# Kernel tuning notes

Hardware: AMD Instinct MI355X
Metric: run time of the kernel (lower is better)

The kernel has to match this reference:

```python
import jax, jax.numpy as jnp
import numpy as np

D_MODEL = 512
PROJ = 2 * D_MODEL  # 1024
N_STATES = 32
KSIZE = 4
LN_EPS = 1e-3  # keras LayerNormalization default epsilon


def setup_inputs() -> dict:
    key = jax.random.key(0)
    ks = jax.random.split(key, 16)
    B, L = 2, 2048
    s_in = 1.0 / np.sqrt(D_MODEL)
    s_pr = 1.0 / np.sqrt(PROJ)
    x = jax.random.normal(ks[0], (B, L, D_MODEL), dtype=jnp.float32)
    # LayerNorm params
    ln_gamma = jnp.ones((D_MODEL,), jnp.float32)
    ln_beta = jnp.zeros((D_MODEL,), jnp.float32)
    # dense1 / dense2: d_model -> proj
    W1 = jax.random.normal(ks[1], (D_MODEL, PROJ), jnp.float32) * s_in
    b1 = jnp.zeros((PROJ,), jnp.float32)
    W2 = jax.random.normal(ks[2], (D_MODEL, PROJ), jnp.float32) * s_in
    b2 = jnp.zeros((PROJ,), jnp.float32)
    # depthwise causal conv1d: kernel (K, 1, PROJ) in WIO layout, groups=PROJ
    conv_k = jax.random.normal(ks[3], (KSIZE, 1, PROJ), jnp.float32) * 0.5
    conv_b = jnp.zeros((PROJ,), jnp.float32)
    # SSM params
    A_log = jnp.log(jnp.broadcast_to(jnp.arange(1, N_STATES + 1, dtype=jnp.float32), (PROJ, N_STATES)))
    D_skip = jnp.ones((PROJ,), jnp.float32)
    WB = jax.random.normal(ks[4], (PROJ, N_STATES), jnp.float32) * s_pr
    bB = jnp.zeros((N_STATES,), jnp.float32)
    WC = jax.random.normal(ks[5], (PROJ, N_STATES), jnp.float32) * s_pr
    bC = jnp.zeros((N_STATES,), jnp.float32)
    Wd = jax.random.normal(ks[6], (PROJ, PROJ), jnp.float32) * s_pr
    bd = jnp.zeros((PROJ,), jnp.float32)
    # dense3: proj -> d_model
    W3 = jax.random.normal(ks[7], (PROJ, D_MODEL), jnp.float32) * s_pr
    b3 = jnp.zeros((D_MODEL,), jnp.float32)
    return dict(x=x, ln_gamma=ln_gamma, ln_beta=ln_beta, W1=W1, b1=b1, W2=W2, b2=b2,
                conv_k=conv_k, conv_b=conv_b, A_log=A_log, D_skip=D_skip,
                WB=WB, bB=bB, WC=WC, bC=bC, Wd=Wd, bd=bd, W3=W3, b3=b3)


def _layernorm(x, gamma, beta):
    mu = jnp.mean(x, axis=-1, keepdims=True)
    var = jnp.mean(jnp.square(x - mu), axis=-1, keepdims=True)
    return (x - mu) * jax.lax.rsqrt(var + LN_EPS) * gamma + beta


def _causal_dwconv(x, k, b):
    # x: [B,L,C], k: [K,1,C], depthwise causal conv (left-pad K-1)
    y = jax.lax.conv_general_dilated(
        x, k, window_strides=(1,), padding=[(KSIZE - 1, 0)],
        dimension_numbers=('NWC', 'WIO', 'NWC'), feature_group_count=PROJ)
    return y + b


def _selective_scan(u, delta, A, Bm, Cm, D_skip):
    # u, delta: [B,L,D]; A: [D,N]; Bm, Cm: [B,L,N]; D_skip: [D]
    deltaA = jnp.einsum('bld,dn->bldn', delta, A)                 # [B,L,D,N]
    deltaBu = jnp.einsum('bld,bld,bln->bldn', delta, u, Bm)        # [B,L,D,N]
    # shift deltaA left by one along L, zero at the end (pad trick in source)
    shifted = jnp.concatenate([deltaA[:, 1:], jnp.zeros_like(deltaA[:, :1])], axis=1)
    # reversed cumsum along L, then exp
    e = jnp.exp(jnp.flip(jnp.cumsum(jnp.flip(shifted, axis=1), axis=1), axis=1))
    xs = jnp.cumsum(deltaBu * e, axis=1) / (e + 1e-12)
    y = jnp.einsum('bldn,bln->bld', xs, Cm)
    return y + u * D_skip


def reference(x, ln_gamma, ln_beta, W1, b1, W2, b2, conv_k, conv_b,
              A_log, D_skip, WB, bB, WC, bC, Wd, bd, W3, b3):
    h = _layernorm(x, ln_gamma, ln_beta)
    x1 = h @ W1 + b1                      # [B,L,PROJ]
    x1 = _causal_dwconv(x1, conv_k, conv_b)
    x1 = jax.nn.silu(x1)
    A = -jnp.exp(A_log)                    # [PROJ,N]
    Cm = x1 @ WC + bC                      # [B,L,N]
    Bm = x1 @ WB + bB                      # [B,L,N]
    delta = jax.nn.softplus(x1 @ Wd + bd)  # [B,L,PROJ]
    y = _selective_scan(x1, delta, A, Bm, Cm, D_skip)
    x2 = jax.nn.silu(h @ W2 + b2)
    out = (y * x2) @ W3 + b3 + x           # residual; dropout is identity at inference
    return out
```

## Files before the change

### kernel.cpp

```cpp
#include <hip/hip_runtime.h>
#include <stdint.h>

#define L_SEQ 2048
#define BATCH 2
#define DMODEL 512
#define PROJ 1024
#define NST 32
#define NCATU 1088
#define ROWS (BATCH*L_SEQ)
#define THRESH 50.0f

typedef float f32x4 __attribute__((ext_vector_type(4)));
typedef short short8 __attribute__((ext_vector_type(8)));

__device__ inline float bf2f(unsigned short u){ uint32_t x=((uint32_t)u)<<16; float f; __builtin_memcpy(&f,&x,4); return f; }
__device__ inline unsigned short f2bf(float f){ uint32_t x; __builtin_memcpy(&x,&f,4); uint32_t r=x+0x7FFFu+((x>>16)&1u); return (unsigned short)(r>>16); }
__device__ inline float siluf(float x){ return x/(1.f+__expf(-x)); }
__device__ inline float softplusf(float x){ return x>20.f? x : log1pf(__expf(x)); }

#define AS1(p) ((const __attribute__((address_space(1))) void*)(p))
#define AS3(p) ((__attribute__((address_space(3))) void*)(p))

template<int N> __device__ inline void wait_vmcnt(){
  if constexpr (N==0)      asm volatile("s_waitcnt vmcnt(0)" ::: "memory");
  else if constexpr (N==4) asm volatile("s_waitcnt vmcnt(4)" ::: "memory");
  else if constexpr (N==8) asm volatile("s_waitcnt vmcnt(8)" ::: "memory");
  else                     asm volatile("s_waitcnt vmcnt(12)" ::: "memory");
}

__global__ __launch_bounds__(256)
void prep_ln_kernel(const float* __restrict__ W1, const float* __restrict__ b1,
                    const float* __restrict__ W2, const float* __restrict__ b2,
                    const float* __restrict__ Wd, const float* __restrict__ bd,
                    const float* __restrict__ WB, const float* __restrict__ bB,
                    const float* __restrict__ WC, const float* __restrict__ bC,
                    const float* __restrict__ W3,
                    unsigned short* __restrict__ W12t, unsigned short* __restrict__ Wcatt,
                    unsigned short* __restrict__ W3t, float* __restrict__ bias12,
                    float* __restrict__ biascat,
                    const float* __restrict__ x, const float* __restrict__ ln_g,
                    const float* __restrict__ ln_b, unsigned short* __restrict__ H)
{
  __shared__ float tile[32][33];
  int bid = blockIdx.x;
  int lx = threadIdx.x & 31, ly = threadIdx.x >> 5;
  if (bid < 1024) {
    int kt = bid & 15, nt = bid >> 4;
    int k0 = kt*32, n0 = nt*32;
    const float* S = (n0 < 1024) ? W1 : W2;
    int nc = (n0 < 1024) ? n0 : n0 - 1024;
#pragma unroll
    for (int i=0;i<4;i++)
      tile[ly+i*8][lx] = S[(size_t)(k0+ly+i*8)*1024 + nc + lx];
    __syncthreads();
#pragma unroll
    for (int i=0;i<4;i++)
      W12t[(size_t)(n0+ly+i*8)*512 + k0 + lx] = f2bf(tile[lx][ly+i*8]);
    return;
  }
  if (bid < 2112) {
    int t = bid - 1024;
    int kt = t & 31, nt = t >> 5;
    int k0 = kt*32, n0 = nt*32;
#pragma unroll
    for (int i=0;i<4;i++){
      int k = k0 + ly + i*8;
      float v;
      if (n0 < 1024)       v = Wd[(size_t)k*1024 + n0 + lx];
      else if (n0 == 1024) v = WB[(size_t)k*32 + lx];
      else                 v = WC[(size_t)k*32 + lx];
      tile[ly+i*8][lx] = v;
    }
    __syncthreads();
#pragma unroll
    for (int i=0;i<4;i++)
      Wcatt[(size_t)(n0+ly+i*8)*1024 + k0 + lx] = f2bf(tile[lx][ly+i*8]);
    return;
  }
  if (bid < 2624) {
    int t = bid - 2112;
    int kt = t & 31, nt = t >> 5;
    int k0 = kt*32, n0 = nt*32;
#pragma unroll
    for (int i=0;i<4;i++)
      tile[ly+i*8][lx] = W3[(size_t)(k0+ly+i*8)*512 + n0 + lx];
    __syncthreads();
#pragma unroll
    for (int i=0;i<4;i++)
      W3t[(size_t)(n0+ly+i*8)*1024 + k0 + lx] = f2bf(tile[lx][ly+i*8]);
    return;
  }
  if (bid < 2637) {
    int j = (bid - 2624)*256 + threadIdx.x;
    if (j < 2048) { bias12[j] = (j < 1024) ? b1[j] : b2[j-1024]; return; }
    j -= 2048;
    if (j < NCATU) biascat[j] = (j < 1024) ? bd[j] : (j < 1056) ? bB[j-1024] : bC[j-1056];
    return;
  }
  int row = (bid - 2637)*4 + (threadIdx.x >> 6);
  int lane = threadIdx.x & 63;
  const float4* xr = (const float4*)(x + (size_t)row*DMODEL);
  float4 v0 = xr[lane];
  float4 v1 = xr[lane+64];
  float s = v0.x+v0.y+v0.z+v0.w + v1.x+v1.y+v1.z+v1.w;
  float q = v0.x*v0.x+v0.y*v0.y+v0.z*v0.z+v0.w*v0.w
          + v1.x*v1.x+v1.y*v1.y+v1.z*v1.z+v1.w*v1.w;
#pragma unroll
  for (int m=32;m>0;m>>=1){ s += __shfl_xor(s,m); q += __shfl_xor(q,m); }
  float mu = s*(1.f/DMODEL);
  float var = q*(1.f/DMODEL) - mu*mu;
  float rs = rsqrtf(var + 1e-3f);
  int c0 = lane*4, c1 = 256 + lane*4;
  float4 g0 = *(const float4*)&ln_g[c0]; float4 g1 = *(const float4*)&ln_g[c1];
  float4 t0 = *(const float4*)&ln_b[c0]; float4 t1 = *(const float4*)&ln_b[c1];
  ushort4 o0, o1;
  o0.x = f2bf((v0.x-mu)*rs*g0.x + t0.x);
  o0.y = f2bf((v0.y-mu)*rs*g0.y + t0.y);
  o0.z = f2bf((v0.z-mu)*rs*g0.z + t0.z);
  o0.w = f2bf((v0.w-mu)*rs*g0.w + t0.w);
  o1.x = f2bf((v1.x-mu)*rs*g1.x + t1.x);
  o1.y = f2bf((v1.y-mu)*rs*g1.y + t1.y);
  o1.z = f2bf((v1.z-mu)*rs*g1.z + t1.z);
  o1.w = f2bf((v1.w-mu)*rs*g1.w + t1.w);
  *(ushort4*)&H[(size_t)row*DMODEL + c0] = o0;
  *(ushort4*)&H[(size_t)row*DMODEL + c1] = o1;
}

template<int MODE>
__global__ __launch_bounds__(256)
void gemm64(const unsigned short* __restrict__ A, const unsigned short* __restrict__ Bt,
            void* __restrict__ Cv, void* __restrict__ Cv2, const float* __restrict__ bias,
            int M, int N, int K, int Kfull)
{
  constexpr int BK = 64;
  constexpr int LPT = 4;
  __shared__ unsigned short As[3][64*BK];
  __shared__ unsigned short Bs[3][64*BK];
  int tid = threadIdx.x;
  int lane = tid & 63, wid = tid >> 6;
  int wm = wid >> 1, wn = wid & 1;
  int gx = gridDim.x;
  int nwg = gx * gridDim.y;
  int L = blockIdx.y*gx + blockIdx.x;
  int W = (L & 7)*(nwg >> 3) + (L >> 3);
  int bx = W % gx, by = W / gx;
  int m0 = bx*64, n0 = by*64;
  int kofs = blockIdx.z*K;

  f32x4 acc[2][2];
#pragma unroll
  for (int i=0;i<2;i++)
#pragma unroll
    for (int j=0;j<2;j++)
#pragma unroll
      for (int e=0;e<4;e++) acc[i][j][e] = 0.f;

  const unsigned short* ap[2];
  const unsigned short* bp[2];
#pragma unroll
  for (int j=0;j<2;j++){
    int s = tid + j*256;
    int row = s >> 3, kc = ((s & 7) ^ (row & 7)) * 8;
    ap[j] = A + (size_t)(m0+row)*Kfull + kofs + kc;
    bp[j] = Bt + (size_t)(n0+row)*Kfull + kofs + kc;
  }
  auto stage = [&](int buf){
#pragma unroll
    for (int j=0;j<2;j++){
      __builtin_amdgcn_global_load_lds(AS1(ap[j]), AS3(&As[buf][(size_t)(j*256 + wid*64)*8]), 16, 0, 0);
      ap[j] += BK;
    }
#pragma unroll
    for (int j=0;j<2;j++){
      __builtin_amdgcn_global_load_lds(AS1(bp[j]), AS3(&Bs[buf][(size_t)(j*256 + wid*64)*8]), 16, 0, 0);
      bp[j] += BK;
    }
  };
  stage(0); stage(1);
  int T = K/BK;
  int rb = 0, wb = 2;
  int r = lane & 15, kb = lane >> 4;
  for (int t = 0; t < T; ++t) {
    if (t+1 < T) wait_vmcnt<LPT>();
    else         wait_vmcnt<0>();
    __builtin_amdgcn_s_barrier();
    if (t+2 < T) { stage(wb); wb = (wb==2)?0:wb+1; }
#pragma unroll
    for (int ks=0; ks<2; ++ks) {
      int cx = (ks*4 + kb) ^ (r & 7);
      short8 af[2], bfr[2];
#pragma unroll
      for (int i=0;i<2;i++) af[i]  = *(const short8*)&As[rb][((wm*32 + i*16 + r)*8 + cx)*8];
#pragma unroll
      for (int j=0;j<2;j++) bfr[j] = *(const short8*)&Bs[rb][((wn*32 + j*16 + r)*8 + cx)*8];
      __builtin_amdgcn_s_setprio(1);
#pragma unroll
      for (int i=0;i<2;i++)
#pragma unroll
        for (int j=0;j<2;j++)
          acc[i][j] = __builtin_amdgcn_mfma_f32_16x16x32_bf16(af[i], bfr[j], acc[i][j], 0,0,0);
      __builtin_amdgcn_s_setprio(0);
    }
    rb = (rb==2)?0:rb+1;
  }
  int rr = (lane >> 4)*4, cc = lane & 15;
#pragma unroll
  for (int i=0;i<2;i++)
#pragma unroll
    for (int j=0;j<2;j++) {
      int col = n0 + wn*32 + j*16 + cc;
#pragma unroll
      for (int e=0;e<4;e++) {
        int row = m0 + wm*32 + i*16 + rr + e;
        float v = acc[i][j][e];
        if constexpr (MODE == 1) {
          v += bias[col];
          if (col < 1024) ((unsigned short*)Cv)[(size_t)row*1024 + col] = f2bf(v);
          else            ((unsigned short*)Cv2)[(size_t)row*1024 + col - 1024] = f2bf(siluf(v));
        } else if constexpr (MODE == 2) {
          v += bias[row];
          if (row < 1024) v = softplusf(v);
          ((float*)Cv)[(size_t)row*N + col] = v;
        } else {
          ((float*)Cv)[(size_t)blockIdx.z*M*N + (size_t)row*N + col] = v;
        }
      }
    }
}

__global__ __launch_bounds__(256)
void reduce_kernel(const float* __restrict__ P, const float* __restrict__ x,
                   const float* __restrict__ b3, float* __restrict__ out)
{
  size_t i = ((size_t)blockIdx.x*256 + threadIdx.x)*4;
  int col = (int)(i & 511);
  float4 a = *(const float4*)&P[i];
  float4 b = *(const float4*)&P[(size_t)ROWS*512 + i];
  float4 xv = *(const float4*)&x[i];
  float4 bv = *(const float4*)&b3[col];
  float4 o;
  o.x = a.x + b.x + xv.x + bv.x;
  o.y = a.y + b.y + xv.y + bv.y;
  o.z = a.z + b.z + xv.z + bv.z;
  o.w = a.w + b.w + xv.w + bv.w;
  *(float4*)&out[i] = o;
}

__global__ __launch_bounds__(256)
void conv_silu_kernel(const unsigned short* __restrict__ P12n, const float* __restrict__ ck,
                      const float* __restrict__ cb, unsigned short* __restrict__ ubf)
{
  int gid = blockIdx.x*256 + threadIdx.x;
  int c = (gid & 255)*4;
  int row = gid >> 8;
  int l = row & (L_SEQ-1);
  float4 bv = *(const float4*)&cb[c];
  float r0=bv.x, r1=bv.y, r2=bv.z, r3=bv.w;
#pragma unroll
  for (int t=0;t<4;t++){
    int lsrc = l - 3 + t;
    if (lsrc >= 0) {
      ushort4 xv = *(const ushort4*)&P12n[(size_t)(row-3+t)*1024 + c];
      float4 kv = *(const float4*)&ck[t*PROJ + c];
      r0 = fmaf(bf2f(xv.x),kv.x,r0);
      r1 = fmaf(bf2f(xv.y),kv.y,r1);
      r2 = fmaf(bf2f(xv.z),kv.z,r2);
      r3 = fmaf(bf2f(xv.w),kv.w,r3);
    }
  }
  ushort4 o;
  o.x=f2bf(siluf(r0)); o.y=f2bf(siluf(r1)); o.z=f2bf(siluf(r2)); o.w=f2bf(siluf(r3));
  *(ushort4*)&ubf[(size_t)row*PROJ + c] = o;
}

__global__ __launch_bounds__(256)
void utrans_kernel(const unsigned short* __restrict__ u, const unsigned short* __restrict__ x2,
                   unsigned short* __restrict__ uT, unsigned short* __restrict__ x2T)
{
  __shared__ unsigned short tile[32][33];
  const unsigned short* src = blockIdx.z ? x2 : u;
  unsigned short* dst = blockIdx.z ? x2T : uT;
  int r0 = blockIdx.x*32, c0 = blockIdx.y*32;
  int lx = threadIdx.x & 31, ly = threadIdx.x >> 5;
#pragma unroll
  for (int i=0;i<4;i++)
    tile[ly+i*8][lx] = src[(size_t)(r0+ly+i*8)*1024 + c0 + lx];
  __syncthreads();
#pragma unroll
  for (int i=0;i<4;i++)
    dst[(size_t)(c0+ly+i*8)*ROWS + r0 + lx] = tile[lx][ly+i*8];
}

__global__ __launch_bounds__(256)
void zmul_pre_kernel(const unsigned short* __restrict__ ubf, const unsigned short* __restrict__ x2bf,
                     const float* __restrict__ Dskip, unsigned short* __restrict__ zbf)
{
  size_t i = ((size_t)blockIdx.x*256 + threadIdx.x)*4;
  int d = (int)(i & (PROJ-1));
  ushort4 uu = *(const ushort4*)&ubf[i];
  ushort4 xx = *(const ushort4*)&x2bf[i];
  float4 Dv = *(const float4*)&Dskip[d];
  ushort4 o;
  o.x = f2bf(bf2f(uu.x)*Dv.x*bf2f(xx.x));
  o.y = f2bf(bf2f(uu.y)*Dv.y*bf2f(xx.y));
  o.z = f2bf(bf2f(uu.z)*Dv.z*bf2f(xx.z));
  o.w = f2bf(bf2f(uu.w)*Dv.w*bf2f(xx.w));
  *(ushort4*)&zbf[i] = o;
}

__global__ __launch_bounds__(256)
void sscan_kernel(const float* __restrict__ CT, const unsigned short* __restrict__ uT,
                  const unsigned short* __restrict__ x2T, const float* __restrict__ Dskip,
                  const float* __restrict__ A_log, unsigned short* __restrict__ zbf)
{
  int tid = threadIdx.x;
  int lane = tid & 63;
  int G = blockIdx.x*4 + (tid >> 6);
  int b = G >> 10, d = G & 1023;
  const float* dT = CT + (size_t)d*ROWS + b*L_SEQ;

  float4 v4[8];
#pragma unroll
  for (int it=0; it<8; ++it) v4[it] = *(const float4*)&dT[lane*32 + it*4];
  float p1 = v4[0].x+v4[0].y+v4[0].z+v4[0].w + v4[1].x+v4[1].y+v4[1].z+v4[1].w;
  float p2 = p1 + v4[2].x+v4[2].y+v4[2].z+v4[2].w + v4[3].x+v4[3].y+v4[3].z+v4[3].w;
  float p3 = p2 + v4[4].x+v4[4].y+v4[4].z+v4[4].w + v4[5].x+v4[5].y+v4[5].z+v4[5].w;
  float lsum = p3 + v4[6].x+v4[6].y+v4[6].z+v4[6].w + v4[7].x+v4[7].y+v4[7].z+v4[7].w;
  float incl = lsum;
#pragma unroll
  for (int dlt=1; dlt<64; dlt<<=1){ float t = __shfl_up(incl, dlt, 64); if (lane >= dlt) incl += t; }
  float Tot = __shfl(incl, 63, 64);
  float excl = incl - lsum;
  float bnd0 = Tot - excl;
  float bnd1 = Tot - (excl + p1);
  float bnd2 = Tot - (excl + p2);
  float bnd3 = Tot - (excl + p3);
  int cnt = 0;
  {
    float run = excl;
    const float* vf = (const float*)v4;
#pragma unroll
    for (int i=0;i<32;i++){ cnt += (Tot - run >= THRESH) ? 1 : 0; run += vf[i]; }
  }
#pragma unroll
  for (int m=32;m>0;m>>=1) cnt += __shfl_xor(cnt, m, 64);
  int l0 = cnt > 0 ? cnt-1 : 0;
  int base = l0 & ~7;

  int n = lane & 31;
  float np1 = __expf(A_log[d*NST + n]);
  float Ds = Dskip[d];
  const float* Br = CT + (size_t)(1024+n)*ROWS + b*L_SEQ;
  const float* Cr = CT + (size_t)(1056+n)*ROWS + b*L_SEQ;
  const unsigned short* ub = uT  + (size_t)d*ROWS + b*L_SEQ;
  const unsigned short* xb = x2T + (size_t)d*ROWS + b*L_SEQ;
  unsigned short* zb = zbf + (size_t)b*L_SEQ*PROJ + d;
  float s = 0.f;
  for (int l = base; l < L_SEQ; l += 8) {
    int j = l >> 3, owner = j >> 2, q = j & 3;
    float bsel = (q==0) ? bnd0 : (q==1) ? bnd1 : (q==2) ? bnd2 : bnd3;
    float sufv = __shfl(bsel, owner, 64);
    float4 d0 = *(const float4*)&dT[l];
    float4 d1 = *(const float4*)&dT[l+4];
    float4 B0 = *(const float4*)&Br[l];
    float4 B1 = *(const float4*)&Br[l+4];
    float4 C0 = *(const float4*)&Cr[l];
    float4 C1 = *(const float4*)&Cr[l+4];
    ushort4 u0 = *(const ushort4*)&ub[l], u1 = *(const ushort4*)&ub[l+4];
    ushort4 x0 = *(const ushort4*)&xb[l], x1 = *(const ushort4*)&xb[l+4];
    float dl[8] = {d0.x,d0.y,d0.z,d0.w,d1.x,d1.y,d1.z,d1.w};
    float Bv[8] = {B0.x,B0.y,B0.z,B0.w,B1.x,B1.y,B1.z,B1.w};
    float Cv[8] = {C0.x,C0.y,C0.z,C0.w,C1.x,C1.y,C1.z,C1.w};
    float uu[8] = {bf2f(u0.x),bf2f(u0.y),bf2f(u0.z),bf2f(u0.w),
                   bf2f(u1.x),bf2f(u1.y),bf2f(u1.z),bf2f(u1.w)};
    float xx[8] = {bf2f(x0.x),bf2f(x0.y),bf2f(x0.z),bf2f(x0.w),
                   bf2f(x1.x),bf2f(x1.y),bf2f(x1.z),bf2f(x1.w)};
    float c8[8];
    float cum = 0.f;
#pragma unroll
    for (int t=0;t<8;t++){
      cum += dl[t];
      float decay = __expf(-dl[t]*np1);
      s = fmaf(decay, s, dl[t]*uu[t]*Bv[t]);
      float gte = 1.f/(1.f + 1e-12f*__expf(np1*(sufv - cum)));
      c8[t] = s*gte*Cv[t];
    }
#pragma unroll
    for (int m=16;m>0;m>>=1){
#pragma unroll
      for (int t=0;t<8;t++) c8[t] += __shfl_xor(c8[t], m);
    }
    if (lane == 0) {
#pragma unroll
      for (int t=0;t<8;t++)
        zb[(size_t)(l+t)*PROJ] = f2bf((c8[t] + uu[t]*Ds)*xx[t]);
    }
  }
}

extern "C" void kernel_launch(void* const* d_in, const int* in_sizes, int n_in,
                              void* d_out, int out_size, void* d_ws, size_t ws_size,
                              hipStream_t stream)
{
  const float* x     = (const float*)d_in[0];
  const float* ln_g  = (const float*)d_in[1];
  const float* ln_b  = (const float*)d_in[2];
  const float* W1    = (const float*)d_in[3];
  const float* b1    = (const float*)d_in[4];
  const float* W2    = (const float*)d_in[5];
  const float* b2    = (const float*)d_in[6];
  const float* convk = (const float*)d_in[7];
  const float* convb = (const float*)d_in[8];
  const float* A_log = (const float*)d_in[9];
  const float* Dskip = (const float*)d_in[10];
  const float* WB    = (const float*)d_in[11];
  const float* bB    = (const float*)d_in[12];
  const float* WC    = (const float*)d_in[13];
  const float* bC    = (const float*)d_in[14];
  const float* Wd    = (const float*)d_in[15];
  const float* bd    = (const float*)d_in[16];
  const float* W3    = (const float*)d_in[17];
  const float* b3    = (const float*)d_in[18];

  char* w = (char*)d_ws;
  auto alloc = [&](size_t bytes){ char* p = w; w += (bytes + 255) & ~(size_t)255; return p; };
  unsigned short* Hbf    = (unsigned short*)alloc((size_t)ROWS*DMODEL*2);
  unsigned short* W12t   = (unsigned short*)alloc((size_t)2048*512*2);
  unsigned short* Wcatt  = (unsigned short*)alloc((size_t)NCATU*1024*2);
  unsigned short* W3t    = (unsigned short*)alloc((size_t)512*1024*2);
  float*          bias12 = (float*)alloc(2048*4);
  float*          biascat= (float*)alloc(NCATU*4);
  unsigned short* P12n   = (unsigned short*)alloc((size_t)ROWS*1024*2);
  unsigned short* ubf    = (unsigned short*)alloc((size_t)ROWS*PROJ*2);
  unsigned short* x2bf   = (unsigned short*)alloc((size_t)ROWS*PROJ*2);
  unsigned short* uT     = (unsigned short*)alloc((size_t)PROJ*ROWS*2);
  unsigned short* x2T    = (unsigned short*)alloc((size_t)PROJ*ROWS*2);
  float*          CT     = (float*)alloc((size_t)NCATU*ROWS*4);
  unsigned short* zbf    = (unsigned short*)alloc((size_t)ROWS*PROJ*2);
  float*          Pp     = (float*)alloc((size_t)2*ROWS*512*4);

  prep_ln_kernel<<<3661, 256, 0, stream>>>(W1,b1,W2,b2,Wd,bd,WB,bB,WC,bC,W3,
                                           W12t,Wcatt,W3t,bias12,biascat,
                                           x, ln_g, ln_b, Hbf);

  dim3 g1(ROWS/64, 2048/64);
  gemm64<1><<<g1, 256, 0, stream>>>(Hbf, W12t, P12n, x2bf, bias12, ROWS, 2048, DMODEL, DMODEL);

  conv_silu_kernel<<<ROWS*256/256, 256, 0, stream>>>(P12n, convk, convb, ubf);

  dim3 gt(ROWS/32, PROJ/32, 2);
  utrans_kernel<<<gt, 256, 0, stream>>>(ubf, x2bf, uT, x2T);

  zmul_pre_kernel<<<(ROWS*PROJ/4)/256, 256, 0, stream>>>(ubf, x2bf, Dskip, zbf);

  dim3 g2(NCATU/64, ROWS/64);
  gemm64<2><<<g2, 256, 0, stream>>>(Wcatt, ubf, CT, nullptr, biascat, NCATU, ROWS, PROJ, PROJ);

  sscan_kernel<<<512, 256, 0, stream>>>(CT, uT, x2T, Dskip, A_log, zbf);

  dim3 g3(ROWS/64, 512/64, 2);
  gemm64<5><<<g3, 256, 0, stream>>>(zbf, W3t, Pp, nullptr, b3, ROWS, 512, 512, PROJ);
  reduce_kernel<<<(ROWS*512/4)/256, 256, 0, stream>>>(Pp, x, b3, (float*)d_out);
}
```

Measured before the change: 144.1 us.

## Stream one GEMM operand directly into registers, stage only the other in LDS

```diff
diff --git a/kernel.cpp b/kernel.cpp
--- a/kernel.cpp
+++ b/kernel.cpp
@@ -23,9 +23,8 @@
 
 template<int N> __device__ inline void wait_vmcnt(){
   if constexpr (N==0)      asm volatile("s_waitcnt vmcnt(0)" ::: "memory");
-  else if constexpr (N==4) asm volatile("s_waitcnt vmcnt(4)" ::: "memory");
-  else if constexpr (N==8) asm volatile("s_waitcnt vmcnt(8)" ::: "memory");
-  else                     asm volatile("s_waitcnt vmcnt(12)" ::: "memory");
+  else if constexpr (N==6) asm volatile("s_waitcnt vmcnt(6)" ::: "memory");
+  else                     asm volatile("s_waitcnt vmcnt(8)" ::: "memory");
 }
 
 __global__ __launch_bounds__(256)
@@ -126,16 +125,14 @@
   *(ushort4*)&H[(size_t)row*DMODEL + c1] = o1;
 }
 
-template<int MODE>
+template<int MODE, int REGOP>
 __global__ __launch_bounds__(256)
 void gemm64(const unsigned short* __restrict__ A, const unsigned short* __restrict__ Bt,
             void* __restrict__ Cv, void* __restrict__ Cv2, const float* __restrict__ bias,
             int M, int N, int K, int Kfull)
 {
   constexpr int BK = 64;
-  constexpr int LPT = 4;
-  __shared__ unsigned short As[3][64*BK];
-  __shared__ unsigned short Bs[3][64*BK];
+  __shared__ unsigned short Ls[3][64*BK];
   int tid = threadIdx.x;
   int lane = tid & 63, wid = tid >> 6;
   int wm = wid >> 1, wn = wid & 1;
@@ -155,54 +152,76 @@
 #pragma unroll
       for (int e=0;e<4;e++) acc[i][j][e] = 0.f;
 
-  const unsigned short* ap[2];
-  const unsigned short* bp[2];
+  const unsigned short* Sbase = (REGOP == 0) ? A : Bt;
+  int sOfs = (REGOP == 0) ? m0 : n0;
+  const unsigned short* sp[2];
 #pragma unroll
   for (int j=0;j<2;j++){
     int s = tid + j*256;
     int row = s >> 3, kc = ((s & 7) ^ (row & 7)) * 8;
-    ap[j] = A + (size_t)(m0+row)*Kfull + kofs + kc;
-    bp[j] = Bt + (size_t)(n0+row)*Kfull + kofs + kc;
+    sp[j] = Sbase + (size_t)(sOfs+row)*Kfull + kofs + kc;
   }
   auto stage = [&](int buf){
 #pragma unroll
     for (int j=0;j<2;j++){
-      __builtin_amdgcn_global_load_lds(AS1(ap[j]), AS3(&As[buf][(size_t)(j*256 + wid*64)*8]), 16, 0, 0);
-      ap[j] += BK;
-    }
-#pragma unroll
-    for (int j=0;j<2;j++){
-      __builtin_amdgcn_global_load_lds(AS1(bp[j]), AS3(&Bs[buf][(size_t)(j*256 + wid*64)*8]), 16, 0, 0);
-      bp[j] += BK;
+      __builtin_amdgcn_global_load_lds(AS1(sp[j]), AS3(&Ls[buf][(size_t)(j*256 + wid*64)*8]), 16, 0, 0);
+      sp[j] += BK;
     }
   };
-  stage(0); stage(1);
+
+  int r = lane & 15, kb = lane >> 4;
+  const unsigned short* Rbase = (REGOP == 0) ? Bt : A;
+  int rOfs = (REGOP == 0) ? (n0 + wn*32) : (m0 + wm*32);
+  auto loadR = [&](int t, short8* dst){
+#pragma unroll
+    for (int j=0;j<2;j++)
+#pragma unroll
+      for (int ks=0; ks<2; ++ks)
+        dst[j*2+ks] = *(const short8*)&Rbase[(size_t)(rOfs + j*16 + r)*Kfull + kofs + t*BK + (ks*4+kb)*8];
+  };
+
+  stage(0);
+  stage(1);
+  __builtin_amdgcn_sched_barrier(0);
+  short8 rc[4], rn[4];
+  loadR(0, rc);
+  __builtin_amdgcn_sched_barrier(0);
   int T = K/BK;
-  int rb = 0, wb = 2;
-  int r = lane & 15, kb = lane >> 4;
+  int wb = 2;
   for (int t = 0; t < T; ++t) {
-    if (t+1 < T) wait_vmcnt<LPT>();
-    else         wait_vmcnt<0>();
+    int rb = t % 3;
+    wait_vmcnt<6>();
     __builtin_amdgcn_s_barrier();
     if (t+2 < T) { stage(wb); wb = (wb==2)?0:wb+1; }
+    if (t+1 < T) loadR(t+1, rn);
+    short8 lf[2][2];
 #pragma unroll
     for (int ks=0; ks<2; ++ks) {
       int cx = (ks*4 + kb) ^ (r & 7);
-      short8 af[2], bfr[2];
-#pragma unroll
-      for (int i=0;i<2;i++) af[i]  = *(const short8*)&As[rb][((wm*32 + i*16 + r)*8 + cx)*8];
-#pragma unroll
-      for (int j=0;j<2;j++) bfr[j] = *(const short8*)&Bs[rb][((wn*32 + j*16 + r)*8 + cx)*8];
-      __builtin_amdgcn_s_setprio(1);
+      int lrow = (REGOP == 0) ? (wm*32) : (wn*32);
 #pragma unroll
       for (int i=0;i<2;i++)
-#pragma unroll
-        for (int j=0;j<2;j++)
-          acc[i][j] = __builtin_amdgcn_mfma_f32_16x16x32_bf16(af[i], bfr[j], acc[i][j], 0,0,0);
-      __builtin_amdgcn_s_setprio(0);
-    }
-    rb = (rb==2)?0:rb+1;
-  }
+        lf[ks][i] = *(const short8*)&Ls[rb][((lrow + i*16 + r)*8 + cx)*8];
+    }
+    asm volatile("s_waitcnt lgkmcnt(0)" ::: "memory");
+    __builtin_amdgcn_sched_barrier(0);
+    __builtin_amdgcn_s_setprio(1);
+#pragma unroll
+    for (int ks=0; ks<2; ++ks)
+#pragma unroll
+      for (int i=0;i<2;i++)
+#pragma unroll
+        for (int j=0;j<2;j++){
+          if constexpr (REGOP == 0)
+            acc[i][j] = __builtin_amdgcn_mfma_f32_16x16x32_bf16(lf[ks][i], rc[j*2+ks], acc[i][j], 0,0,0);
+          else
+            acc[i][j] = __builtin_amdgcn_mfma_f32_16x16x32_bf16(rc[i*2+ks], lf[ks][j], acc[i][j], 0,0,0);
+        }
+    __builtin_amdgcn_s_setprio(0);
+#pragma unroll
+    for (int k=0;k<4;k++) rc[k] = rn[k];
+  }
+
   int rr = (lane >> 4)*4, cc = lane & 15;
 #pragma unroll
   for (int i=0;i<2;i++)
@@ -444,7 +463,7 @@
                                            x, ln_g, ln_b, Hbf);
 
   dim3 g1(ROWS/64, 2048/64);
-  gemm64<1><<<g1, 256, 0, stream>>>(Hbf, W12t, P12n, x2bf, bias12, ROWS, 2048, DMODEL, DMODEL);
+  gemm64<1,0><<<g1, 256, 0, stream>>>(Hbf, W12t, P12n, x2bf, bias12, ROWS, 2048, DMODEL, DMODEL);
 
   conv_silu_kernel<<<ROWS*256/256, 256, 0, stream>>>(P12n, convk, convb, ubf);
 
@@ -454,11 +473,11 @@
   zmul_pre_kernel<<<(ROWS*PROJ/4)/256, 256, 0, stream>>>(ubf, x2bf, Dskip, zbf);
 
   dim3 g2(NCATU/64, ROWS/64);
-  gemm64<2><<<g2, 256, 0, stream>>>(Wcatt, ubf, CT, nullptr, biascat, NCATU, ROWS, PROJ, PROJ);
+  gemm64<2,1><<<g2, 256, 0, stream>>>(Wcatt, ubf, CT, nullptr, biascat, NCATU, ROWS, PROJ, PROJ);
 
   sscan_kernel<<<512, 256, 0, stream>>>(CT, uT, x2T, Dskip, A_log, zbf);
 
   dim3 g3(ROWS/64, 512/64, 2);
-  gemm64<5><<<g3, 256, 0, stream>>>(zbf, W3t, Pp, nullptr, b3, ROWS, 512, 512, PROJ);
+  gemm64<5,0><<<g3, 256, 0, stream>>>(zbf, W3t, Pp, nullptr, b3, ROWS, 512, 512, PROJ);
   reduce_kernel<<<(ROWS*512/4)/256, 256, 0, stream>>>(Pp, x, b3, (float*)d_out);
 }
```

Result: slower. 179.9 us (+24.9%).
